# Kernel optimization log

Measured on AMD Instinct MI355X. Metric: run time of the kernel, lower is better.

## Reference

```python
import jax, jax.numpy as jnp
import numpy as np

V, E, H, A, L = 32000, 512, 1024, 1024, 2
B, T, S = 16, 64, 64


def gru_cell(x, h, W_ih, W_hh, b_ih, b_hh):
    # torch GRUCell math: gates ordered (r, z, n)
    gx = x @ W_ih.T + b_ih
    gh = h @ W_hh.T + b_hh
    xr, xz, xn = jnp.split(gx, 3, axis=-1)
    hr, hz, hn = jnp.split(gh, 3, axis=-1)
    r = jax.nn.sigmoid(xr + hr)
    z = jax.nn.sigmoid(xz + hz)
    n = jnp.tanh(xn + r * hn)
    return (1.0 - z) * n + z * h


def setup_inputs() -> dict:
    key = jax.random.key(0)
    ks = jax.random.split(key, 20)
    s = 0.02
    return {
        "tgt": jax.random.randint(ks[0], (B, T), 0, V),
        "hidden": jax.random.normal(ks[1], (L, B, H), jnp.float32) * 0.1,
        "encoder_outputs": jax.random.normal(ks[2], (B, S, H), jnp.float32),
        "emb": jax.random.normal(ks[3], (V, E), jnp.float32) * s,
        "Wq": jax.random.normal(ks[4], (H, A), jnp.float32) * s,
        "Wk": jax.random.normal(ks[5], (H, A), jnp.float32) * s,
        "v_att": jax.random.normal(ks[6], (A,), jnp.float32) * s,
        "W_ih0": jax.random.normal(ks[7], (3 * H, E + H), jnp.float32) * s,
        "W_hh0": jax.random.normal(ks[8], (3 * H, H), jnp.float32) * s,
        "b_ih0": jnp.zeros((3 * H,), jnp.float32),
        "b_hh0": jnp.zeros((3 * H,), jnp.float32),
        "W_ih1": jax.random.normal(ks[9], (3 * H, H), jnp.float32) * s,
        "W_hh1": jax.random.normal(ks[10], (3 * H, H), jnp.float32) * s,
        "b_ih1": jnp.zeros((3 * H,), jnp.float32),
        "b_hh1": jnp.zeros((3 * H,), jnp.float32),
        "W_out": jax.random.normal(ks[11], (V, H), jnp.float32) * s,
        "b_out": jnp.zeros((V,), jnp.float32),
    }


def reference(tgt, hidden, encoder_outputs, emb, Wq, Wk, v_att,
              W_ih0, W_hh0, b_ih0, b_hh0, W_ih1, W_hh1, b_ih1, b_hh1,
              W_out, b_out):
    # Teacher forcing (ratio=1.0), dropout in eval mode (identity).
    keys_proj = jnp.einsum('bsh,ha->bsa', encoder_outputs, Wk)  # precompute W_k K
    emb_tok = emb[tgt]  # [B,T,E]

    def step(carry, x_t):
        h0, h1 = carry  # each [B,H]
        # Bahdanau attention: query = last-layer hidden
        q = jnp.einsum('bh,ha->ba', h1, Wq)
        scores = jnp.einsum('bsa,a->bs', jnp.tanh(q[:, None, :] + keys_proj), v_att)
        attn = jax.nn.softmax(scores, axis=-1)
        ctx = jnp.einsum('bs,bsh->bh', attn, encoder_outputs)
        rnn_in = jnp.concatenate([x_t, ctx], axis=-1)  # [B, E+H]
        h0n = gru_cell(rnn_in, h0, W_ih0, W_hh0, b_ih0, b_hh0)
        h1n = gru_cell(h0n, h1, W_ih1, W_hh1, b_ih1, b_hh1)
        logits = h1n @ W_out.T + b_out  # [B,V]
        return (h0n, h1n), logits

    (_, _), logits = jax.lax.scan(step, (hidden[0], hidden[1]),
                                  jnp.swapaxes(emb_tok, 0, 1))  # xs: [T,B,E]
    return jnp.swapaxes(logits, 0, 1)  # [B,T,V]
```

## Files before the change

kernel.cpp:

```cpp
#include <hip/hip_runtime.h>
#include <hip/hip_bf16.h>
#include <math.h>

typedef __bf16 bf16x8 __attribute__((ext_vector_type(8)));
typedef float  f32x4  __attribute__((ext_vector_type(4)));

#define MFMA16 __builtin_amdgcn_mfma_f32_16x16x32_bf16
#define WAIT_VM0()   { asm volatile("s_waitcnt vmcnt(0)" ::: "memory");   __builtin_amdgcn_sched_barrier(0); }
#define WAIT_LGKM0() { asm volatile("s_waitcnt lgkmcnt(0)" ::: "memory"); __builtin_amdgcn_sched_barrier(0); }

__device__ __forceinline__ float sigm(float x){ return 1.0f/(1.0f+expf(-x)); }
__device__ __forceinline__ f32x4 ld4(const float* p){ return *(const f32x4*)p; }
__device__ __forceinline__ void split2(float x, __bf16* h, __bf16* l){
  __bf16 hh = (__bf16)x; *h = hh; *l = (__bf16)(x - (float)hh);
}

__global__ __launch_bounds__(256) void k_transpose(const float* __restrict__ in,
                                                   float* __restrict__ out, int R, int C){
  __shared__ float tile[32][33];
  int c0 = blockIdx.x*32, r0 = blockIdx.y*32;
  int tx = threadIdx.x & 31, ty = threadIdx.x >> 5;
  for(int i=ty;i<32;i+=8) tile[i][tx] = in[(size_t)(r0+i)*C + c0+tx];
  __syncthreads();
  for(int i=ty;i<32;i+=8) out[(size_t)(c0+i)*R + r0+tx] = tile[tx][i];
}

__global__ __launch_bounds__(256) void k_gather(const int* __restrict__ tgt,
                                                const float* __restrict__ emb,
                                                float* __restrict__ emb_tok){
  int m = blockIdx.x;
  int t = m >> 4, b = m & 15;
  int row = tgt[b*64 + t];
  const float* src = emb + (size_t)row*512;
  float* dst = emb_tok + (size_t)m*512;
  for(int e=threadIdx.x;e<512;e+=256) dst[e] = src[e];
}

__global__ __launch_bounds__(256) void k_gemm_s(
    const float* __restrict__ A, int lda,
    const float* __restrict__ Bt, int ldb,
    const float* __restrict__ bias,
    float* __restrict__ C, int N, int K)
{
  __shared__ __align__(16) __bf16 Ash[128][40];
  __shared__ __align__(16) __bf16 Asl[128][40];
  __shared__ __align__(16) __bf16 Bsh[64][40];
  __shared__ __align__(16) __bf16 Bsl[64][40];
  int tid = threadIdx.x;
  int m0 = blockIdx.x*128, n0 = blockIdx.y*64;
  int lane = tid & 63, wave = tid >> 6;
  int wr = wave >> 1, wc = wave & 1;
  int qq = lane >> 4, rr = lane & 15;
  f32x4 acc[4][2] = {};
  int ar = tid >> 1, ak = (tid & 1)*16;
  int br = tid >> 2, bk = (tid & 3)*8;
  for(int k0=0;k0<K;k0+=32){
    const float* ap = A + (size_t)(m0+ar)*lda + k0 + ak;
    f32x4 a0 = ld4(ap), a1 = ld4(ap+4), a2 = ld4(ap+8), a3 = ld4(ap+12);
    const float* bp = Bt + (size_t)(n0+br)*ldb + k0 + bk;
    f32x4 b0 = ld4(bp), b1 = ld4(bp+4);
    __syncthreads();
    #pragma unroll
    for(int e=0;e<4;++e){
      split2(a0[e], &Ash[ar][ak+e],    &Asl[ar][ak+e]);
      split2(a1[e], &Ash[ar][ak+4+e],  &Asl[ar][ak+4+e]);
      split2(a2[e], &Ash[ar][ak+8+e],  &Asl[ar][ak+8+e]);
      split2(a3[e], &Ash[ar][ak+12+e], &Asl[ar][ak+12+e]);
      split2(b0[e], &Bsh[br][bk+e],    &Bsl[br][bk+e]);
      split2(b1[e], &Bsh[br][bk+4+e],  &Bsl[br][bk+4+e]);
    }
    __syncthreads();
    bf16x8 afh[4], afl[4], bfh[2], bfl[2];
    #pragma unroll
    for(int mi=0;mi<4;++mi){
      afh[mi] = *(const bf16x8*)&Ash[wr*64 + mi*16 + rr][qq*8];
      afl[mi] = *(const bf16x8*)&Asl[wr*64 + mi*16 + rr][qq*8];
    }
    #pragma unroll
    for(int ni=0;ni<2;++ni){
      bfh[ni] = *(const bf16x8*)&Bsh[wc*32 + ni*16 + rr][qq*8];
      bfl[ni] = *(const bf16x8*)&Bsl[wc*32 + ni*16 + rr][qq*8];
    }
    #pragma unroll
    for(int mi=0;mi<4;++mi)
      #pragma unroll
      for(int ni=0;ni<2;++ni){
        acc[mi][ni] = MFMA16(afh[mi], bfh[ni], acc[mi][ni], 0,0,0);
        acc[mi][ni] = MFMA16(afl[mi], bfh[ni], acc[mi][ni], 0,0,0);
        acc[mi][ni] = MFMA16(afh[mi], bfl[ni], acc[mi][ni], 0,0,0);
      }
  }
  #pragma unroll
  for(int mi=0;mi<4;++mi)
    #pragma unroll
    for(int ni=0;ni<2;++ni)
      #pragma unroll
      for(int i=0;i<4;++i){
        int m = m0 + wr*64 + mi*16 + qq*4 + i;
        int n = n0 + wc*32 + ni*16 + rr;
        C[(size_t)m*N + n] = acc[mi][ni][i] + (bias? bias[n] : 0.f);
      }
}

__global__ __launch_bounds__(256) void k_pack_w(const float* __restrict__ W,
                                                __bf16* __restrict__ Wp){
  int jt = blockIdx.x, tid = threadIdx.x;
  #pragma unroll
  for(int it=0; it<8; ++it){
    int pos = it*256 + tid;
    int kt = pos>>6, l = pos&63;
    const float* src = W + (size_t)(jt*16 + (l&15))*1024 + kt*32 + (l>>4)*8;
    f32x4 s0 = ld4(src), s1 = ld4(src+4);
    bf16x8 vh, vl;
    #pragma unroll
    for(int e=0;e<4;++e){
      __bf16 h, lo;
      split2(s0[e], &h, &lo); vh[e]   = h; vl[e]   = lo;
      split2(s1[e], &h, &lo); vh[4+e] = h; vl[4+e] = lo;
    }
    __bf16* dst = Wp + ((size_t)(jt*32 + kt))*1024 + l*8;
    *(bf16x8*)dst       = vh;
    *(bf16x8*)(dst+512) = vl;
  }
}

__global__ __launch_bounds__(256) void k_pack_wT(const float* __restrict__ W, int ldw,
                                                 __bf16* __restrict__ Wp){
  int jt = blockIdx.x, tid = threadIdx.x;
  #pragma unroll
  for(int it=0; it<8; ++it){
    int pos = it*256 + tid;
    int kt = pos>>6, l = pos&63;
    int j = jt*16 + (l&15);
    int kbase = kt*32 + (l>>4)*8;
    bf16x8 vh, vl;
    #pragma unroll
    for(int e=0;e<8;++e){
      float x = W[(size_t)(kbase+e)*ldw + j];
      __bf16 h = (__bf16)x;
      vh[e] = h; vl[e] = (__bf16)(x - (float)h);
    }
    __bf16* dst = Wp + ((size_t)(jt*32 + kt))*1024 + l*8;
    *(bf16x8*)dst       = vh;
    *(bf16x8*)(dst+512) = vl;
  }
}

__global__ __launch_bounds__(256) void k_split_h(const float* __restrict__ hidden,
    __bf16* __restrict__ h0h, __bf16* __restrict__ h0l,
    __bf16* __restrict__ h1h, __bf16* __restrict__ h1l){
  int i = blockIdx.x*256 + threadIdx.x;
  float x = hidden[i];
  if(i < 16384) split2(x, &h0h[i], &h0l[i]);
  else { int j = i - 16384; split2(x, &h1h[j], &h1l[j]); }
}

__global__ __launch_bounds__(256) void k_cvt16(const float* __restrict__ in,
                                               __bf16* __restrict__ out){
  int i = blockIdx.x*256 + threadIdx.x;
  const float* p = in + (size_t)i*8;
  f32x4 f0 = ld4(p), f1 = ld4(p+4);
  bf16x8 v;
  #pragma unroll
  for(int e=0;e<4;++e){ v[e] = (__bf16)f0[e]; v[4+e] = (__bf16)f1[e]; }
  *(bf16x8*)(out + (size_t)i*8) = v;
}

__device__ __forceinline__ void stage_tile(const __bf16* __restrict__ Wp, int jt,
                                           char* stage, int w, int lane){
  const char* gsrc = (const char*)Wp + (size_t)jt*65536 + (size_t)w*8192 + lane*16;
  char* ldst = stage + w*8192;
  #pragma unroll
  for(int i=0;i<8;++i)
    __builtin_amdgcn_global_load_lds(
      (const __attribute__((address_space(1))) unsigned int*)(gsrc + i*1024),
      (__attribute__((address_space(3))) unsigned int*)(ldst + i*1024), 16, 0, 0);
}

__device__ __forceinline__ void gemv_lds(const __bf16* __restrict__ hh,
                                         const __bf16* __restrict__ hl,
                                         const __bf16* __restrict__ Wp, int jt,
                                         char* stage, float* __restrict__ out, int ldo){
  int tid = threadIdx.x, lane = tid & 63, w = tid >> 6;
  const __bf16* Ah = hh + (lane&15)*1024 + (lane>>4)*8;
  const __bf16* Al = hl + (lane&15)*1024 + (lane>>4)*8;
  bf16x8 ah[4], al[4];
  #pragma unroll
  for(int kk=0;kk<4;++kk){
    int k0 = (w*4+kk)*32;
    ah[kk] = *(const bf16x8*)(Ah + k0);
    al[kk] = *(const bf16x8*)(Al + k0);
  }
  stage_tile(Wp, jt, stage, w, lane);
  WAIT_VM0();
  f32x4 acc = {0.f,0.f,0.f,0.f};
  #pragma unroll
  for(int kk=0;kk<4;++kk){
    bf16x8 bh = *(const bf16x8*)(stage + w*8192 + kk*2048 + lane*16);
    bf16x8 bl = *(const bf16x8*)(stage + w*8192 + kk*2048 + 1024 + lane*16);
    acc = MFMA16(ah[kk], bh, acc, 0,0,0);
    acc = MFMA16(al[kk], bh, acc, 0,0,0);
    acc = MFMA16(ah[kk], bl, acc, 0,0,0);
  }
  *(f32x4*)(stage + w*8192 + lane*16) = acc;
  __syncthreads();
  if(tid < 64){
    f32x4 s = *(const f32x4*)(stage + tid*16);
    #pragma unroll
    for(int k=1;k<8;++k) s += *(const f32x4*)(stage + k*8192 + tid*16);
    int j = jt*16 + (tid & 15);
    #pragma unroll
    for(int i=0;i<4;++i) out[(size_t)((tid>>4)*4 + i)*ldo + j] = s[i];
  }
}

__global__ __launch_bounds__(512) void k_boot(const __bf16* __restrict__ hh,
                                              const __bf16* __restrict__ hl,
                                              const __bf16* __restrict__ Wp,
                                              float* __restrict__ gh0){
  __shared__ __align__(16) char stage[65536];
  gemv_lds(hh, hl, Wp, blockIdx.x, stage, gh0, 3072);
}

__global__ __launch_bounds__(512) void k_SA(
    const __bf16* __restrict__ h1h, const __bf16* __restrict__ h1l,
    const __bf16* __restrict__ Whh1p, const __bf16* __restrict__ Wqp,
    const float* __restrict__ kp, const float* __restrict__ v_att,
    float* __restrict__ gh1, float* __restrict__ parts)
{
  __shared__ __align__(16) char stage[65536];
  int blk = blockIdx.x, tid = threadIdx.x;
  if(blk < 192){ gemv_lds(h1h, h1l, Whh1p, blk, stage, gh1, 3072); return; }
  int slice = blk - 192;
  int lane = tid & 63, w = tid >> 6;
  {
    const __bf16* Ah = h1h + (lane&15)*1024 + (lane>>4)*8;
    const __bf16* Al = h1l + (lane&15)*1024 + (lane>>4)*8;
    bf16x8 ah[4], al[4];
    #pragma unroll
    for(int kk=0;kk<4;++kk){
      int k0 = (w*4+kk)*32;
      ah[kk] = *(const bf16x8*)(Ah + k0);
      al[kk] = *(const bf16x8*)(Al + k0);
    }
    stage_tile(Wqp, slice, stage, w, lane);
    WAIT_VM0();
    f32x4 acc = {0.f,0.f,0.f,0.f};
    #pragma unroll
    for(int kk=0;kk<4;++kk){
      bf16x8 bh = *(const bf16x8*)(stage + w*8192 + kk*2048 + lane*16);
      bf16x8 bl = *(const bf16x8*)(stage + w*8192 + kk*2048 + 1024 + lane*16);
      acc = MFMA16(ah[kk], bh, acc, 0,0,0);
      acc = MFMA16(al[kk], bh, acc, 0,0,0);
      acc = MFMA16(ah[kk], bl, acc, 0,0,0);
    }
    *(f32x4*)(stage + w*8192 + lane*16) = acc;
    __syncthreads();
    if(tid < 64){
      f32x4 s = *(const f32x4*)(stage + tid*16);
      #pragma unroll
      for(int k=1;k<8;++k) s += *(const f32x4*)(stage + k*8192 + tid*16);
      float* qsp = (float*)(stage + 1024);
      #pragma unroll
      for(int i=0;i<4;++i) qsp[((tid>>4)*4 + i)*16 + (tid&15)] = s[i];
    }
    __syncthreads();
  }
  const float* qsp = (const float*)(stage + 1024);
  const float* vp = v_att + slice*16;
  f32x4 v0 = ld4(vp), v1 = ld4(vp+4), v2 = ld4(vp+8), v3 = ld4(vp+12);
  #pragma unroll
  for(int r=0;r<2;++r){
    int pair = r*512 + tid;
    int b = pair >> 6;
    const float* kpr = kp + (size_t)pair*1024 + slice*16;
    f32x4 c0 = ld4(kpr), c1 = ld4(kpr+4), c2 = ld4(kpr+8), c3 = ld4(kpr+12);
    const float* qb = qsp + b*16;
    float acc = 0.f;
    #pragma unroll
    for(int e=0;e<4;++e){
      acc += v0[e]*tanhf(qb[e]     + c0[e]);
      acc += v1[e]*tanhf(qb[4+e]   + c1[e]);
      acc += v2[e]*tanhf(qb[8+e]   + c2[e]);
      acc += v3[e]*tanhf(qb[12+e]  + c3[e]);
    }
    parts[(size_t)slice*1024 + pair] = acc;
  }
}

__global__ __launch_bounds__(512) void k_SB(int t,
    const float* __restrict__ parts, const float* __restrict__ EW,
    const float* __restrict__ GX0x, const float* __restrict__ gh0,
    const float* __restrict__ b_hh0,
    const float* __restrict__ h0_in, float* __restrict__ h0_out,
    __bf16* __restrict__ h0h, __bf16* __restrict__ h0l)
{
  __shared__ float ssum[256][2];
  __shared__ float sc[4][64];
  __shared__ float sden[4];
  __shared__ float part[8][4][16][3];
  int blk = blockIdx.x, tid = threadIdx.x;
  int jt = blk >> 2, bq = blk & 3;
  {
    int hf = tid >> 8, p = tid & 255;
    int pair = bq*256 + p;
    const float* pp = parts + (size_t)(hf*32)*1024 + pair;
    float s = 0.f;
    #pragma unroll
    for(int k=0;k<32;++k) s += pp[(size_t)k*1024];
    ssum[p][hf] = s;
  }
  __syncthreads();
  if(tid < 256) sc[tid>>6][tid&63] = expf(ssum[tid][0] + ssum[tid][1]);
  __syncthreads();
  if(tid < 4){
    float d = 0.f;
    #pragma unroll
    for(int s2=0;s2<64;++s2) d += sc[tid][s2];
    sden[tid] = d;
  }
  __syncthreads();
  int lane = tid & 63, w = tid >> 6;
  int bl = lane >> 4, jl = lane & 15;
  int b = bq*4 + bl, col = jt*16 + jl;
  float a0=0.f, a1=0.f, a2=0.f;
  const float* ewp = EW + ((size_t)(b*64 + w*8))*3072 + col;
  #pragma unroll
  for(int si=0; si<8; ++si){
    float e = sc[bl][w*8 + si];
    const float* r2 = ewp + (size_t)si*3072;
    a0 += e*r2[0]; a1 += e*r2[1024]; a2 += e*r2[2048];
  }
  part[w][bl][jl][0]=a0; part[w][bl][jl][1]=a1; part[w][bl][jl][2]=a2;
  __syncthreads();
  if(tid < 64){
    int bl2 = tid >> 4, jl2 = tid & 15;
    int b2 = bq*4 + bl2, j = jt*16 + jl2;
    float xr=0.f, xz=0.f, xn=0.f;
    #pragma unroll
    for(int k=0;k<8;++k){ xr+=part[k][bl2][jl2][0]; xz+=part[k][bl2][jl2][1]; xn+=part[k][bl2][jl2][2]; }
    float inv = 1.0f / sden[bl2];
    const float* gx = GX0x + ((size_t)t*16 + b2)*3072 + j;
    const float* g0 = gh0 + (size_t)b2*3072 + j;
    float r = sigm(xr*inv + gx[0]    + g0[0]    + b_hh0[j]);
    float z = sigm(xz*inv + gx[1024] + g0[1024] + b_hh0[1024+j]);
    float n = tanhf(xn*inv + gx[2048] + r*(g0[2048] + b_hh0[2048+j]));
    float hnew = (1.f-z)*n + z*h0_in[b2*1024 + j];
    h0_out[b2*1024 + j] = hnew;
    split2(hnew, &h0h[b2*1024 + j], &h0l[b2*1024 + j]);
  }
}

__global__ __launch_bounds__(512) void k_SC(int t,
    const __bf16* __restrict__ h0h, const __bf16* __restrict__ h0l,
    const __bf16* __restrict__ Wih1p, const __bf16* __restrict__ Whh0p,
    const float* __restrict__ b_ih1, const float* __restrict__ b_hh1,
    const float* __restrict__ gh1,
    const float* __restrict__ h1_in, float* __restrict__ h1_out,
    __bf16* __restrict__ h1h, __bf16* __restrict__ h1l,
    __bf16* __restrict__ Hb, float* __restrict__ gh0)
{
  __shared__ __align__(16) char stage[65536];
  int blk = blockIdx.x, tid = threadIdx.x;
  if(blk >= 64){ gemv_lds(h0h, h0l, Whh0p, blk-64, stage, gh0, 3072); return; }
  int lane = tid & 63, w = tid >> 6;
  const __bf16* Ah = h0h + (lane&15)*1024 + (lane>>4)*8;
  const __bf16* Al = h0l + (lane&15)*1024 + (lane>>4)*8;
  bf16x8 ah[4], al[4];
  #pragma unroll
  for(int kk=0;kk<4;++kk){
    int k0 = (w*4+kk)*32;
    ah[kk] = *(const bf16x8*)(Ah + k0);
    al[kk] = *(const bf16x8*)(Al + k0);
  }
  f32x4 accg[3];
  bf16x8 bh[4], bl[4];
  stage_tile(Wih1p, 0*64 + blk, stage, w, lane);
  #pragma unroll
  for(int g=0; g<3; ++g){
    WAIT_VM0();
    #pragma unroll
    for(int kk=0;kk<4;++kk){
      bh[kk] = *(const bf16x8*)(stage + w*8192 + kk*2048 + lane*16);
      bl[kk] = *(const bf16x8*)(stage + w*8192 + kk*2048 + 1024 + lane*16);
    }
    if(g < 2){
      WAIT_LGKM0();
      stage_tile(Wih1p, (g+1)*64 + blk, stage, w, lane);
    }
    f32x4 acc = {0.f,0.f,0.f,0.f};
    #pragma unroll
    for(int kk=0;kk<4;++kk){
      acc = MFMA16(ah[kk], bh[kk], acc, 0,0,0);
      acc = MFMA16(al[kk], bh[kk], acc, 0,0,0);
      acc = MFMA16(ah[kk], bl[kk], acc, 0,0,0);
    }
    accg[g] = acc;
  }
  #pragma unroll
  for(int g=0; g<3; ++g)
    *(f32x4*)(stage + w*8192 + g*1024 + lane*16) = accg[g];
  __syncthreads();
  float* xgp = (float*)(stage + 4096);
  if(tid < 192){
    int g = tid >> 6, tt = tid & 63;
    f32x4 s = *(const f32x4*)(stage + g*1024 + tt*16);
    #pragma unroll
    for(int k=1;k<8;++k) s += *(const f32x4*)(stage + k*8192 + g*1024 + tt*16);
    #pragma unroll
    for(int i=0;i<4;++i) xgp[g*256 + ((tt>>4)*4 + i)*16 + (tt&15)] = s[i];
  }
  __syncthreads();
  if(tid < 256){
    int b = tid >> 4, jl = tid & 15, j = blk*16 + jl;
    float xr = xgp[0*256 + b*16 + jl] + b_ih1[j];
    float xz = xgp[1*256 + b*16 + jl] + b_ih1[1024+j];
    float xn = xgp[2*256 + b*16 + jl] + b_ih1[2048+j];
    const float* g1 = gh1 + (size_t)b*3072 + j;
    float r = sigm(xr + g1[0]    + b_hh1[j]);
    float z = sigm(xz + g1[1024] + b_hh1[1024+j]);
    float n = tanhf(xn + r*(g1[2048] + b_hh1[2048+j]));
    float hnew = (1.f-z)*n + z*h1_in[b*1024 + j];
    h1_out[b*1024 + j] = hnew;
    split2(hnew, &h1h[b*1024 + j], &h1l[b*1024 + j]);
    Hb[((size_t)t*16 + b)*1024 + j] = (__bf16)hnew;
  }
}

__global__ __launch_bounds__(512) void k_logits(
    const __bf16* __restrict__ Hb, const __bf16* __restrict__ Wb,
    const float* __restrict__ b_out, float* __restrict__ out)
{
  int c = blockIdx.x & 7, j = blockIdx.x >> 3;
  int x = j & 3, y = (j >> 2)*8 + c;
  if(y >= 250) return;
  int tm0 = x*256, tn0 = y*128;
  __shared__ __align__(16) __bf16 As[2][256][40];
  int tid = threadIdx.x;
  int lane = tid & 63, wave = tid >> 6;
  int wr = wave >> 1, wc = wave & 1;
  int qq = lane >> 4, rr = lane & 15;
  f32x4 acc[4][4] = {};
  int ar = tid >> 2, ak = (tid & 3) * 8;
  const __bf16* A0 = Hb + (size_t)(tm0+ar)*1024 + ak;
  const __bf16* A1 = Hb + (size_t)(tm0+128+ar)*1024 + ak;
  bf16x8 sa0 = *(const bf16x8*)A0;
  bf16x8 sa1 = *(const bf16x8*)A1;
  *(bf16x8*)&As[0][ar][ak]     = sa0;
  *(bf16x8*)&As[0][128+ar][ak] = sa1;
  __syncthreads();
  for(int k0=0;k0<1024;k0+=32){
    int cur = (k0>>5)&1;
    bool more = (k0+32) < 1024;
    if(more){
      sa0 = *(const bf16x8*)(A0 + k0+32);
      sa1 = *(const bf16x8*)(A1 + k0+32);
    }
    bf16x8 af[4], bfr[4];
    #pragma unroll
    for(int mi=0;mi<4;++mi) af[mi] = *(const bf16x8*)&As[cur][wr*64 + mi*16 + rr][qq*8];
    #pragma unroll
    for(int ni=0;ni<4;++ni)
      bfr[ni] = *(const bf16x8*)(Wb + (size_t)(tn0 + wc*64 + ni*16 + rr)*1024 + k0 + qq*8);
    #pragma unroll
    for(int mi=0;mi<4;++mi)
      #pragma unroll
      for(int ni=0;ni<4;++ni)
        acc[mi][ni] = MFMA16(af[mi], bfr[ni], acc[mi][ni], 0,0,0);
    if(more){
      *(bf16x8*)&As[cur^1][ar][ak]     = sa0;
      *(bf16x8*)&As[cur^1][128+ar][ak] = sa1;
    }
    __syncthreads();
  }
  #pragma unroll
  for(int mi=0;mi<4;++mi)
    #pragma unroll
    for(int ni=0;ni<4;++ni)
      #pragma unroll
      for(int i=0;i<4;++i){
        int m = tm0 + wr*64 + mi*16 + qq*4 + i;
        int v = tn0 + wc*64 + ni*16 + rr;
        int bb = m & 15, tt = m >> 4;
        out[((size_t)bb*64 + tt)*32000 + v] = acc[mi][ni][i] + b_out[v];
      }
}

extern "C" void kernel_launch(void* const* d_in, const int* in_sizes, int n_in,
                              void* d_out, int out_size, void* d_ws, size_t ws_size,
                              hipStream_t stream){
  const int*   tgt    = (const int*)d_in[0];
  const float* hidden = (const float*)d_in[1];
  const float* enc    = (const float*)d_in[2];
  const float* emb    = (const float*)d_in[3];
  const float* Wq     = (const float*)d_in[4];
  const float* Wk     = (const float*)d_in[5];
  const float* v_att  = (const float*)d_in[6];
  const float* W_ih0  = (const float*)d_in[7];
  const float* W_hh0  = (const float*)d_in[8];
  const float* b_ih0  = (const float*)d_in[9];
  const float* b_hh0  = (const float*)d_in[10];
  const float* W_ih1  = (const float*)d_in[11];
  const float* W_hh1  = (const float*)d_in[12];
  const float* b_ih1  = (const float*)d_in[13];
  const float* b_hh1  = (const float*)d_in[14];
  const float* W_out  = (const float*)d_in[15];
  const float* b_out  = (const float*)d_in[16];
  float* out = (float*)d_out;

  float* ws = (float*)d_ws;
  size_t off = 0;
  auto alloc = [&](size_t n){ float* p = ws + off; off += n; return p; };
  float*  kp     = alloc((size_t)1024*1024);
  float*  GX0x   = alloc((size_t)1024*3072);
  float*  EW     = alloc((size_t)1024*3072);
  __bf16* Whh0p  = (__bf16*)alloc((size_t)3072*1024);
  __bf16* Whh1p  = (__bf16*)alloc((size_t)3072*1024);
  __bf16* Wih1p  = (__bf16*)alloc((size_t)3072*1024);
  __bf16* Wqp    = (__bf16*)alloc((size_t)1024*1024);
  float*  gh0    = alloc((size_t)16*3072);
  float*  gh1    = alloc((size_t)16*3072);
  float*  parts  = alloc((size_t)64*1024);
  float*  h0A    = alloc((size_t)16*1024);
  float*  h0B    = alloc((size_t)16*1024);
  float*  h1A    = alloc((size_t)16*1024);
  float*  h1B    = alloc((size_t)16*1024);
  __bf16* h0sh   = (__bf16*)alloc((size_t)8192);
  __bf16* h0sl   = (__bf16*)alloc((size_t)8192);
  __bf16* h1sh   = (__bf16*)alloc((size_t)8192);
  __bf16* h1sl   = (__bf16*)alloc((size_t)8192);
  float*  Hb_f   = alloc((size_t)512*1024);
  __bf16* Hb     = (__bf16*)Hb_f;
  float*  emb_tok = Hb_f;
  float*  WT      = EW;
  __bf16* Woutb   = (__bf16*)ws;
  (void)ws_size; (void)in_sizes; (void)n_in; (void)out_size;

  k_gather<<<1024,256,0,stream>>>(tgt, emb, emb_tok);
  k_transpose<<<dim3(32,32),256,0,stream>>>(Wk, WT, 1024, 1024);
  k_gemm_s<<<dim3(8,16),256,0,stream>>>(enc,1024, WT,1024, nullptr, kp, 1024, 1024);
  k_gemm_s<<<dim3(8,48),256,0,stream>>>(emb_tok,512, W_ih0,1536, b_ih0, GX0x, 3072, 512);
  k_gemm_s<<<dim3(8,48),256,0,stream>>>(enc,1024, W_ih0+512,1536, nullptr, EW, 3072, 1024);
  k_pack_wT<<<64,256,0,stream>>>(Wq, 1024, Wqp);
  k_pack_w<<<192,256,0,stream>>>(W_hh0, Whh0p);
  k_pack_w<<<192,256,0,stream>>>(W_hh1, Whh1p);
  k_pack_w<<<192,256,0,stream>>>(W_ih1, Wih1p);
  k_split_h<<<128,256,0,stream>>>(hidden, h0sh, h0sl, h1sh, h1sl);
  k_boot<<<192,512,0,stream>>>(h0sh, h0sl, Whh0p, gh0);

  for(int t=0;t<64;++t){
    const float* h0i = (t==0)? hidden            : ((t&1)? h0A : h0B);
    float*       h0o = (t&1)? h0B : h0A;
    const float* h1i = (t==0)? hidden + 16*1024  : ((t&1)? h1A : h1B);
    float*       h1o = (t&1)? h1B : h1A;
    k_SA<<<256,512,0,stream>>>(h1sh, h1sl, Whh1p, Wqp, kp, v_att, gh1, parts);
    k_SB<<<256,512,0,stream>>>(t, parts, EW, GX0x, gh0, b_hh0, h0i, h0o, h0sh, h0sl);
    k_SC<<<256,512,0,stream>>>(t, h0sh, h0sl, Wih1p, Whh0p, b_ih1, b_hh1, gh1,
                               h1i, h1o, h1sh, h1sl, Hb, gh0);
  }

  k_cvt16<<<16000,256,0,stream>>>(W_out, Woutb);
  k_logits<<<1024,512,0,stream>>>(Hb, Woutb, b_out, out);
}
```

Measured before the change: 2.171 ms.

## Fuse recurrent step kernels into one persistent cooperative kernel with flag barriers

Replaces the 192 per-timestep kernel launches (SA/SB/SC plus boot) with a single cooperative persistent kernel of 256 blocks. Stages inside it are separated by a hand-rolled grid barrier built on a flag array. Global loads and stores of shared state use cache-bypassing sc0/sc1 instructions so blocks see each other's writes. The goal is to remove launch overhead and inter-kernel gaps on the serial recurrence. Separately, the logits GEMM now stages W_out tiles in LDS with a single buffer instead of double-buffering A and reading B directly from global. The risks are barrier spin cost, cache-bypass latency, and correctness depending on all 256 blocks being co-resident.

```diff
diff --git a/kernel.cpp b/kernel.cpp
--- a/kernel.cpp
+++ b/kernel.cpp
@@ -1,9 +1,11 @@
 #include <hip/hip_runtime.h>
+#include <hip/hip_cooperative_groups.h>
 #include <hip/hip_bf16.h>
 #include <math.h>
 
 typedef __bf16 bf16x8 __attribute__((ext_vector_type(8)));
 typedef float  f32x4  __attribute__((ext_vector_type(4)));
+typedef int    i32x4  __attribute__((ext_vector_type(4)));
 
 #define MFMA16 __builtin_amdgcn_mfma_f32_16x16x32_bf16
 #define WAIT_VM0()   { asm volatile("s_waitcnt vmcnt(0)" ::: "memory");   __builtin_amdgcn_sched_barrier(0); }
@@ -13,6 +15,48 @@
 __device__ __forceinline__ f32x4 ld4(const float* p){ return *(const f32x4*)p; }
 __device__ __forceinline__ void split2(float x, __bf16* h, __bf16* l){
   __bf16 hh = (__bf16)x; *h = hh; *l = (__bf16)(x - (float)hh);
+}
+
+__device__ __forceinline__ bf16x8 ldx4b_bf(const __bf16* p){
+  bf16x8 r;
+  asm volatile("global_load_dwordx4 %0, %1, off sc0 sc1" : "=v"(r) : "v"(p) : "memory");
+  return r;
+}
+__device__ __forceinline__ float ldfb(const float* p){
+  float r;
+  asm volatile("global_load_dword %0, %1, off sc0 sc1" : "=v"(r) : "v"(p) : "memory");
+  return r;
+}
+__device__ __forceinline__ void stfb(float* p, float v){
+  asm volatile("global_store_dword %0, %1, off sc0 sc1" :: "v"(p), "v"(v) : "memory");
+}
+__device__ __forceinline__ void stib(int* p, int v){
+  asm volatile("global_store_dword %0, %1, off sc0 sc1" :: "v"(p), "v"(v) : "memory");
+}
+__device__ __forceinline__ void stsb(__bf16* p, __bf16 v){
+  unsigned int b = (unsigned int)__builtin_bit_cast(unsigned short, v);
+  asm volatile("global_store_short %0, %1, off sc0 sc1" :: "v"(p), "v"(b) : "memory");
+}
+
+__device__ __forceinline__ void barrier_dev(int* flags, int blk, int target){
+  WAIT_VM0();
+  __syncthreads();
+  int tid = threadIdx.x;
+  if(tid == 0) stib(flags + blk, target);
+  if(tid < 64){
+    const int* p = flags + tid*4;
+    for(;;){
+      i32x4 v;
+      asm volatile("global_load_dwordx4 %0, %1, off sc0 sc1\n\ts_waitcnt vmcnt(0)"
+                   : "=v"(v) : "v"(p) : "memory");
+      int m01 = v[0] < v[1] ? v[0] : v[1];
+      int m23 = v[2] < v[3] ? v[2] : v[3];
+      int m = m01 < m23 ? m01 : m23;
+      if(__all(m >= target)) break;
+      __builtin_amdgcn_s_sleep(4);
+    }
+  }
+  __syncthreads();
 }
 
 __global__ __launch_bounds__(256) void k_transpose(const float* __restrict__ in,
@@ -166,6 +210,8 @@
   *(bf16x8*)(out + (size_t)i*8) = v;
 }
 
+__global__ void k_init(int* flags){ flags[threadIdx.x] = 0; }
+
 __device__ __forceinline__ void stage_tile(const __bf16* __restrict__ Wp, int jt,
                                            char* stage, int w, int lane){
   const char* gsrc = (const char*)Wp + (size_t)jt*65536 + (size_t)w*8192 + lane*16;
@@ -177,19 +223,17 @@
       (__attribute__((address_space(3))) unsigned int*)(ldst + i*1024), 16, 0, 0);
 }
 
-__device__ __forceinline__ void gemv_lds(const __bf16* __restrict__ hh,
-                                         const __bf16* __restrict__ hl,
+__device__ __forceinline__ void gemv_byp(const __bf16* hh, const __bf16* hl,
                                          const __bf16* __restrict__ Wp, int jt,
-                                         char* stage, float* __restrict__ out, int ldo){
+                                         char* stage, float* out, int ldo){
   int tid = threadIdx.x, lane = tid & 63, w = tid >> 6;
   const __bf16* Ah = hh + (lane&15)*1024 + (lane>>4)*8;
   const __bf16* Al = hl + (lane&15)*1024 + (lane>>4)*8;
   bf16x8 ah[4], al[4];
   #pragma unroll
   for(int kk=0;kk<4;++kk){
-    int k0 = (w*4+kk)*32;
-    ah[kk] = *(const bf16x8*)(Ah + k0);
-    al[kk] = *(const bf16x8*)(Al + k0);
+    ah[kk] = ldx4b_bf(Ah + (w*4+kk)*32);
+    al[kk] = ldx4b_bf(Al + (w*4+kk)*32);
   }
   stage_tile(Wp, jt, stage, w, lane);
   WAIT_VM0();
@@ -210,220 +254,237 @@
     for(int k=1;k<8;++k) s += *(const f32x4*)(stage + k*8192 + tid*16);
     int j = jt*16 + (tid & 15);
     #pragma unroll
-    for(int i=0;i<4;++i) out[(size_t)((tid>>4)*4 + i)*ldo + j] = s[i];
-  }
-}
-
-__global__ __launch_bounds__(512) void k_boot(const __bf16* __restrict__ hh,
-                                              const __bf16* __restrict__ hl,
-                                              const __bf16* __restrict__ Wp,
-                                              float* __restrict__ gh0){
-  __shared__ __align__(16) char stage[65536];
-  gemv_lds(hh, hl, Wp, blockIdx.x, stage, gh0, 3072);
-}
-
-__global__ __launch_bounds__(512) void k_SA(
-    const __bf16* __restrict__ h1h, const __bf16* __restrict__ h1l,
-    const __bf16* __restrict__ Whh1p, const __bf16* __restrict__ Wqp,
-    const float* __restrict__ kp, const float* __restrict__ v_att,
-    float* __restrict__ gh1, float* __restrict__ parts)
-{
-  __shared__ __align__(16) char stage[65536];
+    for(int i=0;i<4;++i) stfb(out + (size_t)((tid>>4)*4 + i)*ldo + j, s[i]);
+  }
+  __syncthreads();
+}
+
+struct RecP {
+  const __bf16 *Whh1p, *Wqp, *Wih1p, *Whh0p;
+  const float *kp, *EW, *GX0x, *v_att;
+  const float *b_hh0, *b_ih1, *b_hh1;
+  const float *hidden;
+  __bf16 *h0h, *h0l, *h1h, *h1l;
+  float *gh0, *gh1, *parts;
+  float *h0A, *h0B, *h1A, *h1B;
+  __bf16 *Hb;
+  int *flags;
+};
+
+__global__ __launch_bounds__(512) void k_rec(RecP P){
+  __shared__ __align__(16) char smem[65536];
   int blk = blockIdx.x, tid = threadIdx.x;
-  if(blk < 192){ gemv_lds(h1h, h1l, Whh1p, blk, stage, gh1, 3072); return; }
-  int slice = blk - 192;
   int lane = tid & 63, w = tid >> 6;
-  {
-    const __bf16* Ah = h1h + (lane&15)*1024 + (lane>>4)*8;
-    const __bf16* Al = h1l + (lane&15)*1024 + (lane>>4)*8;
-    bf16x8 ah[4], al[4];
-    #pragma unroll
-    for(int kk=0;kk<4;++kk){
-      int k0 = (w*4+kk)*32;
-      ah[kk] = *(const bf16x8*)(Ah + k0);
-      al[kk] = *(const bf16x8*)(Al + k0);
-    }
-    stage_tile(Wqp, slice, stage, w, lane);
-    WAIT_VM0();
-    f32x4 acc = {0.f,0.f,0.f,0.f};
-    #pragma unroll
-    for(int kk=0;kk<4;++kk){
-      bf16x8 bh = *(const bf16x8*)(stage + w*8192 + kk*2048 + lane*16);
-      bf16x8 bl = *(const bf16x8*)(stage + w*8192 + kk*2048 + 1024 + lane*16);
-      acc = MFMA16(ah[kk], bh, acc, 0,0,0);
-      acc = MFMA16(al[kk], bh, acc, 0,0,0);
-      acc = MFMA16(ah[kk], bl, acc, 0,0,0);
-    }
-    *(f32x4*)(stage + w*8192 + lane*16) = acc;
-    __syncthreads();
-    if(tid < 64){
-      f32x4 s = *(const f32x4*)(stage + tid*16);
-      #pragma unroll
-      for(int k=1;k<8;++k) s += *(const f32x4*)(stage + k*8192 + tid*16);
-      float* qsp = (float*)(stage + 1024);
-      #pragma unroll
-      for(int i=0;i<4;++i) qsp[((tid>>4)*4 + i)*16 + (tid&15)] = s[i];
-    }
-    __syncthreads();
-  }
-  const float* qsp = (const float*)(stage + 1024);
-  const float* vp = v_att + slice*16;
-  f32x4 v0 = ld4(vp), v1 = ld4(vp+4), v2 = ld4(vp+8), v3 = ld4(vp+12);
-  #pragma unroll
-  for(int r=0;r<2;++r){
-    int pair = r*512 + tid;
-    int b = pair >> 6;
-    const float* kpr = kp + (size_t)pair*1024 + slice*16;
-    f32x4 c0 = ld4(kpr), c1 = ld4(kpr+4), c2 = ld4(kpr+8), c3 = ld4(kpr+12);
-    const float* qb = qsp + b*16;
-    float acc = 0.f;
-    #pragma unroll
-    for(int e=0;e<4;++e){
-      acc += v0[e]*tanhf(qb[e]     + c0[e]);
-      acc += v1[e]*tanhf(qb[4+e]   + c1[e]);
-      acc += v2[e]*tanhf(qb[8+e]   + c2[e]);
-      acc += v3[e]*tanhf(qb[12+e]  + c3[e]);
-    }
-    parts[(size_t)slice*1024 + pair] = acc;
-  }
-}
-
-__global__ __launch_bounds__(512) void k_SB(int t,
-    const float* __restrict__ parts, const float* __restrict__ EW,
-    const float* __restrict__ GX0x, const float* __restrict__ gh0,
-    const float* __restrict__ b_hh0,
-    const float* __restrict__ h0_in, float* __restrict__ h0_out,
-    __bf16* __restrict__ h0h, __bf16* __restrict__ h0l)
-{
-  __shared__ float ssum[256][2];
-  __shared__ float sc[4][64];
-  __shared__ float sden[4];
-  __shared__ float part[8][4][16][3];
-  int blk = blockIdx.x, tid = threadIdx.x;
-  int jt = blk >> 2, bq = blk & 3;
-  {
-    int hf = tid >> 8, p = tid & 255;
-    int pair = bq*256 + p;
-    const float* pp = parts + (size_t)(hf*32)*1024 + pair;
-    float s = 0.f;
-    #pragma unroll
-    for(int k=0;k<32;++k) s += pp[(size_t)k*1024];
-    ssum[p][hf] = s;
-  }
-  __syncthreads();
-  if(tid < 256) sc[tid>>6][tid&63] = expf(ssum[tid][0] + ssum[tid][1]);
-  __syncthreads();
-  if(tid < 4){
-    float d = 0.f;
-    #pragma unroll
-    for(int s2=0;s2<64;++s2) d += sc[tid][s2];
-    sden[tid] = d;
-  }
-  __syncthreads();
-  int lane = tid & 63, w = tid >> 6;
-  int bl = lane >> 4, jl = lane & 15;
-  int b = bq*4 + bl, col = jt*16 + jl;
-  float a0=0.f, a1=0.f, a2=0.f;
-  const float* ewp = EW + ((size_t)(b*64 + w*8))*3072 + col;
-  #pragma unroll
-  for(int si=0; si<8; ++si){
-    float e = sc[bl][w*8 + si];
-    const float* r2 = ewp + (size_t)si*3072;
-    a0 += e*r2[0]; a1 += e*r2[1024]; a2 += e*r2[2048];
-  }
-  part[w][bl][jl][0]=a0; part[w][bl][jl][1]=a1; part[w][bl][jl][2]=a2;
-  __syncthreads();
-  if(tid < 64){
-    int bl2 = tid >> 4, jl2 = tid & 15;
-    int b2 = bq*4 + bl2, j = jt*16 + jl2;
-    float xr=0.f, xz=0.f, xn=0.f;
-    #pragma unroll
-    for(int k=0;k<8;++k){ xr+=part[k][bl2][jl2][0]; xz+=part[k][bl2][jl2][1]; xn+=part[k][bl2][jl2][2]; }
-    float inv = 1.0f / sden[bl2];
-    const float* gx = GX0x + ((size_t)t*16 + b2)*3072 + j;
-    const float* g0 = gh0 + (size_t)b2*3072 + j;
-    float r = sigm(xr*inv + gx[0]    + g0[0]    + b_hh0[j]);
-    float z = sigm(xz*inv + gx[1024] + g0[1024] + b_hh0[1024+j]);
-    float n = tanhf(xn*inv + gx[2048] + r*(g0[2048] + b_hh0[2048+j]));
-    float hnew = (1.f-z)*n + z*h0_in[b2*1024 + j];
-    h0_out[b2*1024 + j] = hnew;
-    split2(hnew, &h0h[b2*1024 + j], &h0l[b2*1024 + j]);
-  }
-}
-
-__global__ __launch_bounds__(512) void k_SC(int t,
-    const __bf16* __restrict__ h0h, const __bf16* __restrict__ h0l,
-    const __bf16* __restrict__ Wih1p, const __bf16* __restrict__ Whh0p,
-    const float* __restrict__ b_ih1, const float* __restrict__ b_hh1,
-    const float* __restrict__ gh1,
-    const float* __restrict__ h1_in, float* __restrict__ h1_out,
-    __bf16* __restrict__ h1h, __bf16* __restrict__ h1l,
-    __bf16* __restrict__ Hb, float* __restrict__ gh0)
-{
-  __shared__ __align__(16) char stage[65536];
-  int blk = blockIdx.x, tid = threadIdx.x;
-  if(blk >= 64){ gemv_lds(h0h, h0l, Whh0p, blk-64, stage, gh0, 3072); return; }
-  int lane = tid & 63, w = tid >> 6;
-  const __bf16* Ah = h0h + (lane&15)*1024 + (lane>>4)*8;
-  const __bf16* Al = h0l + (lane&15)*1024 + (lane>>4)*8;
-  bf16x8 ah[4], al[4];
-  #pragma unroll
-  for(int kk=0;kk<4;++kk){
-    int k0 = (w*4+kk)*32;
-    ah[kk] = *(const bf16x8*)(Ah + k0);
-    al[kk] = *(const bf16x8*)(Al + k0);
-  }
-  f32x4 accg[3];
-  bf16x8 bh[4], bl[4];
-  stage_tile(Wih1p, 0*64 + blk, stage, w, lane);
-  #pragma unroll
-  for(int g=0; g<3; ++g){
-    WAIT_VM0();
-    #pragma unroll
-    for(int kk=0;kk<4;++kk){
-      bh[kk] = *(const bf16x8*)(stage + w*8192 + kk*2048 + lane*16);
-      bl[kk] = *(const bf16x8*)(stage + w*8192 + kk*2048 + 1024 + lane*16);
-    }
-    if(g < 2){
-      WAIT_LGKM0();
-      stage_tile(Wih1p, (g+1)*64 + blk, stage, w, lane);
-    }
-    f32x4 acc = {0.f,0.f,0.f,0.f};
-    #pragma unroll
-    for(int kk=0;kk<4;++kk){
-      acc = MFMA16(ah[kk], bh[kk], acc, 0,0,0);
-      acc = MFMA16(al[kk], bh[kk], acc, 0,0,0);
-      acc = MFMA16(ah[kk], bl[kk], acc, 0,0,0);
-    }
-    accg[g] = acc;
-  }
-  #pragma unroll
-  for(int g=0; g<3; ++g)
-    *(f32x4*)(stage + w*8192 + g*1024 + lane*16) = accg[g];
-  __syncthreads();
-  float* xgp = (float*)(stage + 4096);
-  if(tid < 192){
-    int g = tid >> 6, tt = tid & 63;
-    f32x4 s = *(const f32x4*)(stage + g*1024 + tt*16);
-    #pragma unroll
-    for(int k=1;k<8;++k) s += *(const f32x4*)(stage + k*8192 + g*1024 + tt*16);
-    #pragma unroll
-    for(int i=0;i<4;++i) xgp[g*256 + ((tt>>4)*4 + i)*16 + (tt&15)] = s[i];
-  }
-  __syncthreads();
-  if(tid < 256){
-    int b = tid >> 4, jl = tid & 15, j = blk*16 + jl;
-    float xr = xgp[0*256 + b*16 + jl] + b_ih1[j];
-    float xz = xgp[1*256 + b*16 + jl] + b_ih1[1024+j];
-    float xn = xgp[2*256 + b*16 + jl] + b_ih1[2048+j];
-    const float* g1 = gh1 + (size_t)b*3072 + j;
-    float r = sigm(xr + g1[0]    + b_hh1[j]);
-    float z = sigm(xz + g1[1024] + b_hh1[1024+j]);
-    float n = tanhf(xn + r*(g1[2048] + b_hh1[2048+j]));
-    float hnew = (1.f-z)*n + z*h1_in[b*1024 + j];
-    h1_out[b*1024 + j] = hnew;
-    split2(hnew, &h1h[b*1024 + j], &h1l[b*1024 + j]);
-    Hb[((size_t)t*16 + b)*1024 + j] = (__bf16)hnew;
+
+  if(blk >= 64) gemv_byp(P.h0h, P.h0l, P.Whh0p, blk-64, smem, P.gh0, 3072);
+  barrier_dev(P.flags, blk, 1);
+
+  for(int t=0;t<64;++t){
+    const float* h0i = (t==0)? P.hidden           : ((t&1)? P.h0A : P.h0B);
+    float*       h0o = (t&1)? P.h0B : P.h0A;
+    const float* h1i = (t==0)? P.hidden + 16*1024 : ((t&1)? P.h1A : P.h1B);
+    float*       h1o = (t&1)? P.h1B : P.h1A;
+
+    if(blk < 192){
+      gemv_byp(P.h1h, P.h1l, P.Whh1p, blk, smem, P.gh1, 3072);
+    } else {
+      int slice = blk - 192;
+      const __bf16* Ah = P.h1h + (lane&15)*1024 + (lane>>4)*8;
+      const __bf16* Al = P.h1l + (lane&15)*1024 + (lane>>4)*8;
+      bf16x8 ah[4], al[4];
+      #pragma unroll
+      for(int kk=0;kk<4;++kk){
+        ah[kk] = ldx4b_bf(Ah + (w*4+kk)*32);
+        al[kk] = ldx4b_bf(Al + (w*4+kk)*32);
+      }
+      stage_tile(P.Wqp, slice, smem, w, lane);
+      WAIT_VM0();
+      f32x4 acc = {0.f,0.f,0.f,0.f};
+      #pragma unroll
+      for(int kk=0;kk<4;++kk){
+        bf16x8 bh = *(const bf16x8*)(smem + w*8192 + kk*2048 + lane*16);
+        bf16x8 bl = *(const bf16x8*)(smem + w*8192 + kk*2048 + 1024 + lane*16);
+        acc = MFMA16(ah[kk], bh, acc, 0,0,0);
+        acc = MFMA16(al[kk], bh, acc, 0,0,0);
+        acc = MFMA16(ah[kk], bl, acc, 0,0,0);
+      }
+      *(f32x4*)(smem + w*8192 + lane*16) = acc;
+      __syncthreads();
+      float* qsp = (float*)(smem + 1024);
+      if(tid < 64){
+        f32x4 s = *(const f32x4*)(smem + tid*16);
+        #pragma unroll
+        for(int k=1;k<8;++k) s += *(const f32x4*)(smem + k*8192 + tid*16);
+        #pragma unroll
+        for(int i=0;i<4;++i) qsp[((tid>>4)*4 + i)*16 + (tid&15)] = s[i];
+      }
+      __syncthreads();
+      const float* vp = P.v_att + slice*16;
+      f32x4 v0 = ld4(vp), v1 = ld4(vp+4), v2 = ld4(vp+8), v3 = ld4(vp+12);
+      #pragma unroll
+      for(int r=0;r<2;++r){
+        int pair = r*512 + tid;
+        int b = pair >> 6;
+        const float* kpr = P.kp + (size_t)pair*1024 + slice*16;
+        f32x4 c0 = ld4(kpr), c1 = ld4(kpr+4), c2 = ld4(kpr+8), c3 = ld4(kpr+12);
+        const float* qb = qsp + b*16;
+        float acc2 = 0.f;
+        #pragma unroll
+        for(int e=0;e<4;++e){
+          acc2 += v0[e]*tanhf(qb[e]     + c0[e]);
+          acc2 += v1[e]*tanhf(qb[4+e]   + c1[e]);
+          acc2 += v2[e]*tanhf(qb[8+e]   + c2[e]);
+          acc2 += v3[e]*tanhf(qb[12+e]  + c3[e]);
+        }
+        stfb(P.parts + (size_t)slice*1024 + pair, acc2);
+      }
+    }
+    barrier_dev(P.flags, blk, 3*t+2);
+
+    {
+      float* ssum = (float*)smem;
+      float* scv  = (float*)(smem + 2048);
+      float* sden = (float*)(smem + 3072);
+      float* prt  = (float*)(smem + 3136);
+      int jt = blk >> 2, bq = blk & 3;
+      {
+        int hf = tid >> 8, p = tid & 255;
+        int pair = bq*256 + p;
+        const float* base = P.parts + (size_t)(hf*32)*1024 + pair;
+        float v[32];
+        #pragma unroll
+        for(int k=0;k<32;++k) v[k] = ldfb(base + (size_t)k*1024);
+        WAIT_VM0();
+        float s = 0.f;
+        #pragma unroll
+        for(int k=0;k<32;++k) s += v[k];
+        ssum[p*2 + hf] = s;
+      }
+      __syncthreads();
+      if(tid < 256) scv[(tid>>6)*64 + (tid&63)] = expf(ssum[tid*2] + ssum[tid*2+1]);
+      __syncthreads();
+      if(tid < 4){
+        float d = 0.f;
+        #pragma unroll
+        for(int s2=0;s2<64;++s2) d += scv[tid*64 + s2];
+        sden[tid] = d;
+      }
+      __syncthreads();
+      int bl = lane >> 4, jl = lane & 15;
+      int b = bq*4 + bl, col = jt*16 + jl;
+      float a0=0.f, a1=0.f, a2=0.f;
+      const float* ewp = P.EW + ((size_t)(b*64 + w*8))*3072 + col;
+      #pragma unroll
+      for(int si=0; si<8; ++si){
+        float e = scv[bl*64 + w*8 + si];
+        const float* r2 = ewp + (size_t)si*3072;
+        a0 += e*r2[0]; a1 += e*r2[1024]; a2 += e*r2[2048];
+      }
+      prt[((w*4 + bl)*16 + jl)*3 + 0] = a0;
+      prt[((w*4 + bl)*16 + jl)*3 + 1] = a1;
+      prt[((w*4 + bl)*16 + jl)*3 + 2] = a2;
+      __syncthreads();
+      if(tid < 64){
+        int bl2 = tid >> 4, jl2 = tid & 15;
+        int b2 = bq*4 + bl2, j = jt*16 + jl2;
+        float xr=0.f, xz=0.f, xn=0.f;
+        #pragma unroll
+        for(int k=0;k<8;++k){
+          xr += prt[((k*4 + bl2)*16 + jl2)*3 + 0];
+          xz += prt[((k*4 + bl2)*16 + jl2)*3 + 1];
+          xn += prt[((k*4 + bl2)*16 + jl2)*3 + 2];
+        }
+        float g0r = ldfb(P.gh0 + (size_t)b2*3072 + j);
+        float g0z = ldfb(P.gh0 + (size_t)b2*3072 + 1024 + j);
+        float g0n = ldfb(P.gh0 + (size_t)b2*3072 + 2048 + j);
+        float hprev = ldfb(h0i + b2*1024 + j);
+        WAIT_VM0();
+        float inv = 1.0f / sden[bl2];
+        const float* gx = P.GX0x + ((size_t)t*16 + b2)*3072 + j;
+        float r = sigm(xr*inv + gx[0]    + g0r + P.b_hh0[j]);
+        float z = sigm(xz*inv + gx[1024] + g0z + P.b_hh0[1024+j]);
+        float n = tanhf(xn*inv + gx[2048] + r*(g0n + P.b_hh0[2048+j]));
+        float hnew = (1.f-z)*n + z*hprev;
+        stfb(h0o + b2*1024 + j, hnew);
+        __bf16 hh2, ll2; split2(hnew, &hh2, &ll2);
+        stsb(P.h0h + b2*1024 + j, hh2);
+        stsb(P.h0l + b2*1024 + j, ll2);
+      }
+    }
+    barrier_dev(P.flags, blk, 3*t+3);
+
+    if(blk >= 64){
+      gemv_byp(P.h0h, P.h0l, P.Whh0p, blk-64, smem, P.gh0, 3072);
+    } else {
+      const __bf16* Ah = P.h0h + (lane&15)*1024 + (lane>>4)*8;
+      const __bf16* Al = P.h0l + (lane&15)*1024 + (lane>>4)*8;
+      bf16x8 ah[4], al[4];
+      #pragma unroll
+      for(int kk=0;kk<4;++kk){
+        ah[kk] = ldx4b_bf(Ah + (w*4+kk)*32);
+        al[kk] = ldx4b_bf(Al + (w*4+kk)*32);
+      }
+      f32x4 accg[3];
+      bf16x8 bh[4], bl[4];
+      stage_tile(P.Wih1p, 0*64 + blk, smem, w, lane);
+      WAIT_VM0();
+      #pragma unroll
+      for(int g=0; g<3; ++g){
+        if(g) WAIT_VM0();
+        #pragma unroll
+        for(int kk=0;kk<4;++kk){
+          bh[kk] = *(const bf16x8*)(smem + w*8192 + kk*2048 + lane*16);
+          bl[kk] = *(const bf16x8*)(smem + w*8192 + kk*2048 + 1024 + lane*16);
+        }
+        if(g < 2){
+          WAIT_LGKM0();
+          stage_tile(P.Wih1p, (g+1)*64 + blk, smem, w, lane);
+        }
+        f32x4 acc = {0.f,0.f,0.f,0.f};
+        #pragma unroll
+        for(int kk=0;kk<4;++kk){
+          acc = MFMA16(ah[kk], bh[kk], acc, 0,0,0);
+          acc = MFMA16(al[kk], bh[kk], acc, 0,0,0);
+          acc = MFMA16(ah[kk], bl[kk], acc, 0,0,0);
+        }
+        accg[g] = acc;
+      }
+      #pragma unroll
+      for(int g=0; g<3; ++g)
+        *(f32x4*)(smem + w*8192 + g*1024 + lane*16) = accg[g];
+      __syncthreads();
+      float* xgp = (float*)(smem + 4096);
+      if(tid < 192){
+        int g = tid >> 6, tt = tid & 63;
+        f32x4 s = *(const f32x4*)(smem + g*1024 + tt*16);
+        #pragma unroll
+        for(int k=1;k<8;++k) s += *(const f32x4*)(smem + k*8192 + g*1024 + tt*16);
+        #pragma unroll
+        for(int i=0;i<4;++i) xgp[g*256 + ((tt>>4)*4 + i)*16 + (tt&15)] = s[i];
+      }
+      __syncthreads();
+      if(tid < 256){
+        int b = tid >> 4, jl = tid & 15, j = blk*16 + jl;
+        float g1r = ldfb(P.gh1 + (size_t)b*3072 + j);
+        float g1z = ldfb(P.gh1 + (size_t)b*3072 + 1024 + j);
+        float g1n = ldfb(P.gh1 + (size_t)b*3072 + 2048 + j);
+        float hprev = ldfb(h1i + b*1024 + j);
+        WAIT_VM0();
+        float xr = xgp[0*256 + b*16 + jl] + P.b_ih1[j];
+        float xz = xgp[1*256 + b*16 + jl] + P.b_ih1[1024+j];
+        float xn = xgp[2*256 + b*16 + jl] + P.b_ih1[2048+j];
+        float r = sigm(xr + g1r + P.b_hh1[j]);
+        float z = sigm(xz + g1z + P.b_hh1[1024+j]);
+        float n = tanhf(xn + r*(g1n + P.b_hh1[2048+j]));
+        float hnew = (1.f-z)*n + z*hprev;
+        stfb(h1o + b*1024 + j, hnew);
+        __bf16 hh2, ll2; split2(hnew, &hh2, &ll2);
+        stsb(P.h1h + b*1024 + j, hh2);
+        stsb(P.h1l + b*1024 + j, ll2);
+        P.Hb[((size_t)t*16 + b)*1024 + j] = (__bf16)hnew;
+      }
+    }
+    barrier_dev(P.flags, blk, 3*t+4);
   }
 }
 
@@ -435,43 +496,33 @@
   int x = j & 3, y = (j >> 2)*8 + c;
   if(y >= 250) return;
   int tm0 = x*256, tn0 = y*128;
-  __shared__ __align__(16) __bf16 As[2][256][40];
+  __shared__ __align__(16) __bf16 As[256][40];
+  __shared__ __align__(16) __bf16 Bs[128][40];
   int tid = threadIdx.x;
   int lane = tid & 63, wave = tid >> 6;
   int wr = wave >> 1, wc = wave & 1;
   int qq = lane >> 4, rr = lane & 15;
   f32x4 acc[4][4] = {};
   int ar = tid >> 2, ak = (tid & 3) * 8;
-  const __bf16* A0 = Hb + (size_t)(tm0+ar)*1024 + ak;
-  const __bf16* A1 = Hb + (size_t)(tm0+128+ar)*1024 + ak;
-  bf16x8 sa0 = *(const bf16x8*)A0;
-  bf16x8 sa1 = *(const bf16x8*)A1;
-  *(bf16x8*)&As[0][ar][ak]     = sa0;
-  *(bf16x8*)&As[0][128+ar][ak] = sa1;
-  __syncthreads();
   for(int k0=0;k0<1024;k0+=32){
-    int cur = (k0>>5)&1;
-    bool more = (k0+32) < 1024;
-    if(more){
-      sa0 = *(const bf16x8*)(A0 + k0+32);
-      sa1 = *(const bf16x8*)(A1 + k0+32);
-    }
+    bf16x8 a0v = *(const bf16x8*)(Hb + (size_t)(tm0+ar)*1024     + k0 + ak);
+    bf16x8 a1v = *(const bf16x8*)(Hb + (size_t)(tm0+ar+128)*1024 + k0 + ak);
+    bf16x8 bv  = *(const bf16x8*)(Wb + (size_t)(tn0+ar)*1024     + k0 + ak);
+    __syncthreads();
+    *(bf16x8*)&As[ar][ak]     = a0v;
+    *(bf16x8*)&As[ar+128][ak] = a1v;
+    *(bf16x8*)&Bs[ar][ak]     = bv;
+    __syncthreads();
     bf16x8 af[4], bfr[4];
     #pragma unroll
-    for(int mi=0;mi<4;++mi) af[mi] = *(const bf16x8*)&As[cur][wr*64 + mi*16 + rr][qq*8];
-    #pragma unroll
-    for(int ni=0;ni<4;++ni)
-      bfr[ni] = *(const bf16x8*)(Wb + (size_t)(tn0 + wc*64 + ni*16 + rr)*1024 + k0 + qq*8);
+    for(int mi=0;mi<4;++mi) af[mi]  = *(const bf16x8*)&As[wr*64 + mi*16 + rr][qq*8];
+    #pragma unroll
+    for(int ni=0;ni<4;++ni) bfr[ni] = *(const bf16x8*)&Bs[wc*64 + ni*16 + rr][qq*8];
     #pragma unroll
     for(int mi=0;mi<4;++mi)
       #pragma unroll
       for(int ni=0;ni<4;++ni)
         acc[mi][ni] = MFMA16(af[mi], bfr[ni], acc[mi][ni], 0,0,0);
-    if(more){
-      *(bf16x8*)&As[cur^1][ar][ak]     = sa0;
-      *(bf16x8*)&As[cur^1][128+ar][ak] = sa1;
-    }
-    __syncthreads();
   }
   #pragma unroll
   for(int mi=0;mi<4;++mi)
@@ -530,6 +581,7 @@
   __bf16* h1sh   = (__bf16*)alloc((size_t)8192);
   __bf16* h1sl   = (__bf16*)alloc((size_t)8192);
   float*  Hb_f   = alloc((size_t)512*1024);
+  int*    flags  = (int*)alloc((size_t)256);
   __bf16* Hb     = (__bf16*)Hb_f;
   float*  emb_tok = Hb_f;
   float*  WT      = EW;
@@ -546,18 +598,19 @@
   k_pack_w<<<192,256,0,stream>>>(W_hh1, Whh1p);
   k_pack_w<<<192,256,0,stream>>>(W_ih1, Wih1p);
   k_split_h<<<128,256,0,stream>>>(hidden, h0sh, h0sl, h1sh, h1sl);
-  k_boot<<<192,512,0,stream>>>(h0sh, h0sl, Whh0p, gh0);
-
-  for(int t=0;t<64;++t){
-    const float* h0i = (t==0)? hidden            : ((t&1)? h0A : h0B);
-    float*       h0o = (t&1)? h0B : h0A;
-    const float* h1i = (t==0)? hidden + 16*1024  : ((t&1)? h1A : h1B);
-    float*       h1o = (t&1)? h1B : h1A;
-    k_SA<<<256,512,0,stream>>>(h1sh, h1sl, Whh1p, Wqp, kp, v_att, gh1, parts);
-    k_SB<<<256,512,0,stream>>>(t, parts, EW, GX0x, gh0, b_hh0, h0i, h0o, h0sh, h0sl);
-    k_SC<<<256,512,0,stream>>>(t, h0sh, h0sl, Wih1p, Whh0p, b_ih1, b_hh1, gh1,
-                               h1i, h1o, h1sh, h1sl, Hb, gh0);
-  }
+  k_init<<<1,256,0,stream>>>(flags);
+
+  RecP P;
+  P.Whh1p = Whh1p; P.Wqp = Wqp; P.Wih1p = Wih1p; P.Whh0p = Whh0p;
+  P.kp = kp; P.EW = EW; P.GX0x = GX0x; P.v_att = v_att;
+  P.b_hh0 = b_hh0; P.b_ih1 = b_ih1; P.b_hh1 = b_hh1;
+  P.hidden = hidden;
+  P.h0h = h0sh; P.h0l = h0sl; P.h1h = h1sh; P.h1l = h1sl;
+  P.gh0 = gh0; P.gh1 = gh1; P.parts = parts;
+  P.h0A = h0A; P.h0B = h0B; P.h1A = h1A; P.h1B = h1B;
+  P.Hb = Hb; P.flags = flags;
+  void* args[] = { &P };
+  hipLaunchCooperativeKernel((const void*)k_rec, dim3(256), dim3(512), args, 0, stream);
 
   k_cvt16<<<16000,256,0,stream>>>(W_out, Woutb);
   k_logits<<<1024,512,0,stream>>>(Hb, Woutb, b_out, out);
```

Result: slower. 3.738 ms, median of 2 (+72.2%).
